# Kernel optimization log

Hardware: AMD Instinct MI355X
Metric: run time of the kernel (lower is better)

The kernel has to match this reference:

```python
import jax, jax.numpy as jnp
import numpy as np

COMMITMENT_COST = 0.25


def setup_inputs() -> dict:
    key = jax.random.key(0)
    k1, k2 = jax.random.split(key)
    z = jax.random.normal(k1, (64, 256, 32, 32), dtype=jnp.float32)
    # codebook init ~ U(-1/K, 1/K) as in torch module
    K, D = 1024, 256
    emb = jax.random.uniform(k2, (K, D), dtype=jnp.float32, minval=-1.0 / K, maxval=1.0 / K)
    return {"z": z, "emb": emb}


def reference(z, emb):
    # b c h w -> b h w c
    zt = jnp.transpose(z, (0, 2, 3, 1))
    B, H, W, C = zt.shape
    zf = zt.reshape(-1, C)  # (b*h*w, c)
    # squared euclidean distances: ||z||^2 + ||e||^2 - 2 z.e
    d = (jnp.sum(zf * zf, axis=1, keepdims=True)
         + jnp.sum(emb * emb, axis=1)
         - 2.0 * jnp.einsum('nd,kd->nk', zf, emb))
    min_encoding_indices = jnp.argmin(d, axis=1)  # (b*h*w,)
    z_quantized = emb[min_encoding_indices].reshape(B, H, W, C)
    commitment_loss = COMMITMENT_COST * jnp.mean((jax.lax.stop_gradient(z_quantized) - zt) ** 2)
    codebook_loss = jnp.mean((z_quantized - jax.lax.stop_gradient(zt)) ** 2)
    loss = commitment_loss + codebook_loss
    # straight-through estimator
    z_quantized = zt + jax.lax.stop_gradient(z_quantized - zt)
    out = jnp.transpose(z_quantized, (0, 3, 1, 2))  # b c h w
    return out, loss, min_encoding_indices.reshape(B, H, W)
```

## Files before the change

### kernel.cpp

```cpp
#include <hip/hip_runtime.h>
#include <math.h>

#define KCODES 1024
#define DDIM   256
#define HWSZ   1024
#define CHW    262144
#define LOSS_OFF 16777216
#define IDX_OFF  16777217
#define TAU_GAP  2e-4f
#define RR4      4

#define WS_ZH   0u
#define WS_EH   33554432u
#define WS_EL   34078720u
#define WS_AN   34603008u
#define WS_BN   34865152u
#define WS_LIST 34869248u
#define WS_CNT  35131392u
#define WS_NEED 35131396u

#define OB_ZH   0
#define OB_EH   8388608
#define OB_EL   8519680
#define OB_AN   8650752
#define OB_BN   8716288
#define OB_LIST 8717312
#define OB_CNT  8782848

typedef __attribute__((ext_vector_type(8))) short short8v;
typedef __attribute__((ext_vector_type(4))) float float4v;

#define GLOAD_LDS(gsrc, ldst)                                                   \
    __builtin_amdgcn_global_load_lds(                                           \
        (const __attribute__((address_space(1))) void*)(gsrc),                  \
        (__attribute__((address_space(3))) void*)(ldst), 16, 0, 0)

static __device__ __forceinline__ unsigned short bf16_rne(float f) {
    unsigned u = __float_as_uint(f);
    return (unsigned short)((u + 0x7FFFu + ((u >> 16) & 1u)) >> 16);
}
static __device__ __forceinline__ float bf16_tf(unsigned short h) {
    return __uint_as_float(((unsigned)h) << 16);
}

__global__ __launch_bounds__(64) void vq_prep_bn(const float* __restrict__ emb,
                                                 float* __restrict__ Bn,
                                                 float* __restrict__ loss_slot,
                                                 int* __restrict__ cnt) {
    int k = blockIdx.x * 64 + threadIdx.x;
    if (k == 0) { *cnt = 0; loss_slot[0] = 0.f; }
    if (k >= KCODES) return;
    const float* e = emb + (size_t)k * DDIM;
    float half[2];
    #pragma unroll
    for (int h = 0; h < 2; ++h) {
        const float* q = e + (h << 7);
        float r[8];
        #pragma unroll
        for (int j = 0; j < 8; ++j) r[j] = __fmul_rn(q[j], q[j]);
        for (int i = 8; i < 128; i += 8) {
            #pragma unroll
            for (int j = 0; j < 8; ++j)
                r[j] = __fadd_rn(r[j], __fmul_rn(q[i + j], q[i + j]));
        }
        half[h] = __fadd_rn(
            __fadd_rn(__fadd_rn(r[0], r[1]), __fadd_rn(r[2], r[3])),
            __fadd_rn(__fadd_rn(r[4], r[5]), __fadd_rn(r[6], r[7])));
    }
    Bn[k] = __fadd_rn(half[0], half[1]);
}

__global__ __launch_bounds__(256) void vq_prep_scatter(const float* __restrict__ emb,
                                                       unsigned short* __restrict__ EHg,
                                                       unsigned short* __restrict__ ELg) {
    int task = blockIdx.x * 256 + threadIdx.x;
    int k  = task >> 5;
    int dg = task & 31;
    const float* e = emb + (size_t)k * DDIM + (dg << 3);
    float4 v0 = *(const float4*)e;
    float4 v1 = *(const float4*)(e + 4);
    float f[8] = {v0.x, v0.y, v0.z, v0.w, v1.x, v1.y, v1.z, v1.w};
    short8v hv, lv;
    #pragma unroll
    for (int j = 0; j < 8; ++j) {
        unsigned short hb = bf16_rne(f[j]);
        unsigned short lb = bf16_rne(f[j] - bf16_tf(hb));
        hv[j] = (short)hb; lv[j] = (short)lb;
    }
    int base = ((k >> 4) << 12) + ((dg >> 2) << 9) + (((k & 15) + ((dg & 3) << 4)) << 3);
    *(short8v*)(EHg + base) = hv;
    *(short8v*)(ELg + base) = lv;
}

__global__ __launch_bounds__(256) void vq_zprep2(const float* __restrict__ z,
                                                 unsigned short* __restrict__ ZHg,
                                                 float* __restrict__ An) {
    __shared__ float hs[2][128];
    const int t = threadIdx.x;
    const int nb = blockIdx.x;
    const int b = nb >> 3, hw0 = (nb & 7) << 7;
    const int h = t >> 7, n = t & 127;
    const float* src = z + (size_t)b * CHW + (size_t)(h << 7) * HWSZ + hw0 + n;
    unsigned short* zbase = ZHg + (size_t)nb * 32768 + ((n >> 4) << 9) + ((n & 15) << 3);
    float r[8];
    #pragma unroll
    for (int blk8 = 0; blk8 < 16; ++blk8) {
        float f[8];
        #pragma unroll
        for (int j = 0; j < 8; ++j) f[j] = src[(size_t)((blk8 << 3) + j) * HWSZ];
        if (blk8 == 0) {
            #pragma unroll
            for (int j = 0; j < 8; ++j) r[j] = __fmul_rn(f[j], f[j]);
        } else {
            #pragma unroll
            for (int j = 0; j < 8; ++j) r[j] = __fadd_rn(r[j], __fmul_rn(f[j], f[j]));
        }
        short8v hv;
        #pragma unroll
        for (int j = 0; j < 8; ++j) hv[j] = (short)bf16_rne(f[j]);
        int d = (h << 7) + (blk8 << 3);
        int s32 = d >> 5, g = (d >> 3) & 3;
        *(short8v*)(zbase + s32 * 4096 + (g << 7)) = hv;
    }
    hs[h][n] = __fadd_rn(
        __fadd_rn(__fadd_rn(r[0], r[1]), __fadd_rn(r[2], r[3])),
        __fadd_rn(__fadd_rn(r[4], r[5]), __fadd_rn(r[6], r[7])));
    __syncthreads();
    if (t < 128) An[nb * 128 + t] = __fadd_rn(hs[0][t], hs[1][t]);
}

template<bool WRITE_OUT>
__global__ __launch_bounds__(512, 4) void vq_argmin2g(
        const unsigned short* __restrict__ ZHg,
        const unsigned short* __restrict__ EHg, const unsigned short* __restrict__ ELg,
        const float* __restrict__ An, const float* __restrict__ Bn,
        float* __restrict__ idx_out, int* __restrict__ list, int* __restrict__ cnt,
        float* __restrict__ loss_slot, float* __restrict__ outp,
        const float* __restrict__ emb) {
    __shared__ uint4 ZH4[512];
    __shared__ uint4 EBUF4[2048];
    __shared__ float BNs[1024];
    unsigned short* ZH = (unsigned short*)ZH4;
    unsigned short* EH = (unsigned short*)EBUF4;
    unsigned short* EL = EH + 8192;

    const int t = threadIdx.x;
    const int bid = blockIdx.x;
    const int nb = ((bid & 7) << 6) + (bid >> 3);
    const int b   = nb >> 3;
    const int hw0 = (nb & 7) << 7;
    const int lane = t & 63, w = t >> 6;
    const int kwv = w >> 1, nwv = w & 1;
    const int l8 = lane << 3, g2 = lane >> 4;

    BNs[t] = Bn[t];
    BNs[t + 512] = Bn[t + 512];

    float an[4];
    #pragma unroll
    for (int nf = 0; nf < 4; ++nf)
        an[nf] = An[nb * 128 + nwv * 64 + nf * 16 + (lane & 15)];

    float mv1[4], mv2[4]; int mi1[4];
    #pragma unroll
    for (int i = 0; i < 4; ++i) { mv1[i] = 3.4e38f; mv2[i] = 3.4e38f; mi1[i] = 0x7fffffff; }

    const uint4* zh4 = (const uint4*)ZHg + (size_t)nb * 4096;
    const uint4* eh4 = (const uint4*)EHg;
    const uint4* el4 = (const uint4*)ELg;

    for (int kt = 0; kt < 4; ++kt) {
        float4v acc[4][4];
        #pragma unroll
        for (int a = 0; a < 4; ++a)
            #pragma unroll
            for (int c = 0; c < 4; ++c) acc[a][c] = (float4v){0.f, 0.f, 0.f, 0.f};

        for (int s32 = 0; s32 < 8; ++s32) {
            __syncthreads();
            GLOAD_LDS(zh4 + s32 * 512 + t, &ZH4[t]);
            #pragma unroll
            for (int p = 0; p < 4; ++p) {
                int s = p * 512 + t;
                int arr = s >> 10, ss = s & 1023;
                const uint4* src = (arr ? el4 : eh4)
                    + (size_t)(((kt << 4) + (ss >> 6)) << 9) + (s32 << 6) + (ss & 63);
                uint4* dst = (arr ? ((uint4*)EL) : ((uint4*)EH)) + ss;
                GLOAD_LDS(src, dst);
            }
            __syncthreads();
            short8v ah[4], al[4], bh[4];
            #pragma unroll
            for (int kf = 0; kf < 4; ++kf) {
                int base = ((kwv * 4 + kf) << 9) + l8;
                ah[kf] = *(const short8v*)&EH[base];
                al[kf] = *(const short8v*)&EL[base];
            }
            #pragma unroll
            for (int nf = 0; nf < 4; ++nf)
                bh[nf] = *(const short8v*)&ZH[((nwv * 4 + nf) << 9) + l8];
            #pragma unroll
            for (int kf = 0; kf < 4; ++kf)
                #pragma unroll
                for (int nf = 0; nf < 4; ++nf) {
                    acc[kf][nf] = __builtin_amdgcn_mfma_f32_16x16x32_bf16(ah[kf], bh[nf], acc[kf][nf], 0, 0, 0);
                    acc[kf][nf] = __builtin_amdgcn_mfma_f32_16x16x32_bf16(al[kf], bh[nf], acc[kf][nf], 0, 0, 0);
                }
        }
        #pragma unroll
        for (int kf = 0; kf < 4; ++kf)
            #pragma unroll
            for (int nf = 0; nf < 4; ++nf)
                #pragma unroll
                for (int r = 0; r < 4; ++r) {
                    int k = kt * 256 + kwv * 64 + kf * 16 + g2 * 4 + r;
                    float s = __fsub_rn(__fadd_rn(an[nf], BNs[k]),
                                        __fmul_rn(2.0f, acc[kf][nf][r]));
                    if (s < mv1[nf] || (s == mv1[nf] && k < mi1[nf])) {
                        mv2[nf] = fminf(mv2[nf], mv1[nf]);
                        mv1[nf] = s; mi1[nf] = k;
                    } else if (s < mv2[nf]) mv2[nf] = s;
                }
    }

    __syncthreads();
    float* REDv = (float*)EBUF4;
    int*   REDi = (int*)((char*)EBUF4 + 8192);
    float* REDw = (float*)((char*)EBUF4 + 16384);
    int*   FIDX = (int*)((char*)EBUF4 + 24576);

    #pragma unroll
    for (int nf = 0; nf < 4; ++nf) {
        int nl = nf * 16 + (lane & 15);
        int slot = kwv * 4 + g2;
        REDv[(nwv * 64 + nl) * 16 + slot] = mv1[nf];
        REDi[(nwv * 64 + nl) * 16 + slot] = mi1[nf];
        REDw[(nwv * 64 + nl) * 16 + slot] = mv2[nf];
    }
    __syncthreads();
    if (t < 128) {
        float bv = 3.4e38f, b2 = 3.4e38f; int bi = 0x7fffffff;
        #pragma unroll
        for (int s = 0; s < 16; ++s) {
            float v1 = REDv[t * 16 + s];
            float v2 = REDw[t * 16 + s];
            int   i1 = REDi[t * 16 + s];
            if (v1 < bv || (v1 == bv && i1 < bi)) { b2 = fminf(b2, bv); bv = v1; bi = i1; }
            else b2 = fminf(b2, v1);
            b2 = fminf(b2, v2);
        }
        int n_glob = nb * 128 + t;
        idx_out[n_glob] = (float)bi;
        FIDX[t] = bi;
        if (b2 - bv < TAU_GAP) {
            int pos = atomicAdd(cnt, 1);
            list[pos] = n_glob;
        }
        float lsum = bv;
        #pragma unroll
        for (int off = 32; off > 0; off >>= 1)
            lsum += __shfl_down(lsum, off, 64);
        if ((t & 63) == 0) atomicAdd(loss_slot, lsum * (1.25f / 16777216.f));
    }
    if (WRITE_OUT) {
        __syncthreads();
        int n_loc = t & 127, cg = t >> 7;
        int idx = FIDX[n_loc];
        int hw = hw0 + n_loc;
        const float4* erow = (const float4*)(emb + (size_t)idx * DDIM + (cg << 6));
        float* obase = outp + (size_t)b * CHW + (size_t)(cg << 6) * HWSZ + hw;
        #pragma unroll 4
        for (int q = 0; q < 16; ++q) {
            float4 v = erow[q];
            obase[(size_t)(q * 4 + 0) * HWSZ] = v.x;
            obase[(size_t)(q * 4 + 1) * HWSZ] = v.y;
            obase[(size_t)(q * 4 + 2) * HWSZ] = v.z;
            obase[(size_t)(q * 4 + 3) * HWSZ] = v.w;
        }
    }
}

template<bool WRITE_OUT>
__global__ __launch_bounds__(512) void vq_rescore_c(
        const float* __restrict__ z, const float* __restrict__ emb,
        const float* __restrict__ An, const float* __restrict__ Bn,
        float* __restrict__ idx_out, const int* __restrict__ list,
        const int* __restrict__ cnt, float* __restrict__ outp) {
    const int c = *cnt;
    const int t = threadIdx.x;
    const int lane = t & 63, w = t >> 6;
    const int g  = lane >> 4;
    const int ch = lane & 15;
    __shared__ float zs[RR4][256];
    __shared__ float Ars[RR4];
    __shared__ int   rid[RR4];
    __shared__ float wsv[RR4][8];
    __shared__ int   wsi[RR4][8];
    __shared__ int   wbi[RR4];

    for (int base = blockIdx.x * RR4; base < c; base += gridDim.x * RR4) {
        const int nrows = min(RR4, c - base);
        __syncthreads();
        if (t < nrows) { int n = list[base + t]; rid[t] = n; Ars[t] = An[n]; }
        __syncthreads();
        for (int i = t; i < (nrows << 8); i += 512) {
            int r = i >> 8, d = i & 255;
            int n = rid[r];
            zs[r][d] = z[(size_t)(n >> 10) * CHW + (size_t)d * HWSZ + (n & 1023)];
        }
        __syncthreads();

        float bv[RR4]; int bi[RR4];
        #pragma unroll
        for (int r = 0; r < RR4; ++r) { bv[r] = 3.4e38f; bi[r] = 0x7fffffff; }

        for (int p = 0; p < 32; ++p) {
            int cc = p * 32 + w * 4 + g;
            const float4* e4 = (const float4*)(emb + (size_t)cc * DDIM);
            double part[RR4];
            #pragma unroll
            for (int r = 0; r < RR4; ++r) part[r] = 0.0;
            #pragma unroll
            for (int it = 0; it < 4; ++it) {
                float4 ev = e4[it * 16 + ch];
                #pragma unroll
                for (int r = 0; r < RR4; ++r) {
                    float4 zv = *(const float4*)&zs[r][(it * 16 + ch) << 2];
                    part[r] += (double)ev.x * zv.x + (double)ev.y * zv.y
                             + (double)ev.z * zv.z + (double)ev.w * zv.w;
                }
            }
            #pragma unroll
            for (int off = 1; off <= 8; off <<= 1)
                #pragma unroll
                for (int r = 0; r < RR4; ++r)
                    part[r] += __shfl_xor(part[r], off, 64);
            float Bk = Bn[cc];
            #pragma unroll
            for (int r = 0; r < RR4; ++r) {
                float s = __fsub_rn(__fadd_rn(Ars[r], Bk),
                                    __fmul_rn(2.0f, (float)part[r]));
                if (s < bv[r]) { bv[r] = s; bi[r] = cc; }
            }
        }
        #pragma unroll
        for (int r = 0; r < RR4; ++r) {
            float v = bv[r]; int i1 = bi[r];
            #pragma unroll
            for (int off = 16; off <= 32; off <<= 1) {
                float ov = __shfl_xor(v, off, 64);
                int   oi = __shfl_xor(i1, off, 64);
                if (ov < v || (ov == v && oi < i1)) { v = ov; i1 = oi; }
            }
            if (lane == 0) { wsv[r][w] = v; wsi[r][w] = i1; }
        }
        __syncthreads();
        if (t < nrows) {
            float v = wsv[t][0]; int i1 = wsi[t][0];
            #pragma unroll
            for (int j = 1; j < 8; ++j) {
                float ov = wsv[t][j]; int oi = wsi[t][j];
                if (ov < v || (ov == v && oi < i1)) { v = ov; i1 = oi; }
            }
            idx_out[rid[t]] = (float)i1;
            wbi[t] = i1;
        }
        if (WRITE_OUT) {
            __syncthreads();
            for (int i = t; i < (nrows << 8); i += 512) {
                int r = i >> 8, d = i & 255;
                int n = rid[r];
                outp[(size_t)(n >> 10) * CHW + (size_t)d * HWSZ + (n & 1023)]
                    = emb[(size_t)wbi[r] * DDIM + d];
            }
        }
    }
}

__global__ __launch_bounds__(256) void vq_epilogue(const float* __restrict__ emb,
                                                   float* __restrict__ outp,
                                                   const float* __restrict__ idxf) {
    const int t  = threadIdx.x;
    const int nc = blockIdx.x;
    const int b  = nc >> 4;
    const int hw = ((nc & 15) << 6) + (t & 63);
    const int n  = (b << 10) + hw;
    const int idx = (int)idxf[n];
    const float* erow = emb + (size_t)idx * DDIM;
    const size_t zb = (size_t)b * CHW + hw;

    const int cbase = (t >> 6) << 2;
    #pragma unroll 4
    for (int cq = 0; cq < 16; ++cq) {
        int c = cbase + (cq << 4);
        float4 q4 = *reinterpret_cast<const float4*>(erow + c);
        outp[zb + (size_t)(c + 0) * HWSZ] = q4.x;
        outp[zb + (size_t)(c + 1) * HWSZ] = q4.y;
        outp[zb + (size_t)(c + 2) * HWSZ] = q4.z;
        outp[zb + (size_t)(c + 3) * HWSZ] = q4.w;
    }
}

extern "C" void kernel_launch(void* const* d_in, const int* in_sizes, int n_in,
                              void* d_out, int out_size, void* d_ws, size_t ws_size,
                              hipStream_t stream) {
    const float* z   = (const float*)d_in[0];
    const float* emb = (const float*)d_in[1];
    float* out       = (float*)d_out;
    float* loss_slot = out + LOSS_OFF;
    float* idx_out   = out + IDX_OFF;

    if (ws_size >= (size_t)WS_NEED) {
        char* ws = (char*)d_ws;
        unsigned short* ZHg = (unsigned short*)(ws + WS_ZH);
        unsigned short* EHg = (unsigned short*)(ws + WS_EH);
        unsigned short* ELg = (unsigned short*)(ws + WS_EL);
        float* An = (float*)(ws + WS_AN);
        float* Bn = (float*)(ws + WS_BN);
        int*  list = (int*)(ws + WS_LIST);
        int*  cnt  = (int*)(ws + WS_CNT);

        vq_prep_bn          <<<dim3(16),   dim3(64),  0, stream>>>(emb, Bn, loss_slot, cnt);
        vq_prep_scatter     <<<dim3(128),  dim3(256), 0, stream>>>(emb, EHg, ELg);
        vq_zprep2           <<<dim3(512),  dim3(256), 0, stream>>>(z, ZHg, An);
        vq_argmin2g<true>   <<<dim3(512),  dim3(512), 0, stream>>>(ZHg, EHg, ELg, An, Bn,
                                 idx_out, list, cnt, loss_slot, out, emb);
        vq_rescore_c<true>  <<<dim3(2048), dim3(512), 0, stream>>>(z, emb, An, Bn,
                                 idx_out, list, cnt, out);
    } else {
        unsigned short* ZHg = (unsigned short*)(out + OB_ZH);
        unsigned short* EHg = (unsigned short*)(out + OB_EH);
        unsigned short* ELg = (unsigned short*)(out + OB_EL);
        float* An = out + OB_AN;
        float* Bn = out + OB_BN;
        int*  list = (int*)(out + OB_LIST);
        int*  cnt  = (int*)(out + OB_CNT);

        vq_prep_bn          <<<dim3(16),   dim3(64),  0, stream>>>(emb, Bn, loss_slot, cnt);
        vq_prep_scatter     <<<dim3(128),  dim3(256), 0, stream>>>(emb, EHg, ELg);
        vq_zprep2           <<<dim3(512),  dim3(256), 0, stream>>>(z, ZHg, An);
        vq_argmin2g<false>  <<<dim3(512),  dim3(512), 0, stream>>>(ZHg, EHg, ELg, An, Bn,
                                 idx_out, list, cnt, loss_slot, out, emb);
        vq_rescore_c<false> <<<dim3(2048), dim3(512), 0, stream>>>(z, emb, An, Bn,
                                 idx_out, list, cnt, out);
        vq_epilogue         <<<dim3(1024), dim3(256), 0, stream>>>(emb, out, idx_out);
    }
}
```

Measured before the change: 256.9 us.

## Double-buffer codebook tiles and keep full Z tile resident in LDS

The argmin kernel now loads the entire 128-row bf16 Z tile into shared memory once and double-buffers the codebook hi/lo chunks, so each chunk's global-to-LDS load for the next step overlaps the MFMA work on the current one. This cuts the barrier count per step from two to one. Shared memory per block rises to about 132 KB and launch bounds drop to 2 blocks per CU, which lowers occupancy. The tie-gap threshold for sending rows to the exact rescoring pass is also tightened, so fewer rows are rescored, at some risk of missing near-tie argmins.

```diff
diff --git a/kernel.cpp b/kernel.cpp
--- a/kernel.cpp
+++ b/kernel.cpp
@@ -7,7 +7,7 @@
 #define CHW    262144
 #define LOSS_OFF 16777216
 #define IDX_OFF  16777217
-#define TAU_GAP  2e-4f
+#define TAU_GAP  1.4e-4f
 #define RR4      4
 
 #define WS_ZH   0u
@@ -130,19 +130,17 @@
 }
 
 template<bool WRITE_OUT>
-__global__ __launch_bounds__(512, 4) void vq_argmin2g(
+__global__ __launch_bounds__(512, 2) void vq_argmin2p(
         const unsigned short* __restrict__ ZHg,
         const unsigned short* __restrict__ EHg, const unsigned short* __restrict__ ELg,
         const float* __restrict__ An, const float* __restrict__ Bn,
         float* __restrict__ idx_out, int* __restrict__ list, int* __restrict__ cnt,
         float* __restrict__ loss_slot, float* __restrict__ outp,
         const float* __restrict__ emb) {
-    __shared__ uint4 ZH4[512];
-    __shared__ uint4 EBUF4[2048];
+    __shared__ uint4 ZA4[4096];
+    __shared__ uint4 EB4[2][2048];
     __shared__ float BNs[1024];
-    unsigned short* ZH = (unsigned short*)ZH4;
-    unsigned short* EH = (unsigned short*)EBUF4;
-    unsigned short* EL = EH + 8192;
+    unsigned short* ZA = (unsigned short*)ZA4;
 
     const int t = threadIdx.x;
     const int bid = blockIdx.x;
@@ -153,81 +151,96 @@
     const int kwv = w >> 1, nwv = w & 1;
     const int l8 = lane << 3, g2 = lane >> 4;
 
-    BNs[t] = Bn[t];
-    BNs[t + 512] = Bn[t + 512];
-
-    float an[4];
-    #pragma unroll
-    for (int nf = 0; nf < 4; ++nf)
-        an[nf] = An[nb * 128 + nwv * 64 + nf * 16 + (lane & 15)];
-
-    float mv1[4], mv2[4]; int mi1[4];
-    #pragma unroll
-    for (int i = 0; i < 4; ++i) { mv1[i] = 3.4e38f; mv2[i] = 3.4e38f; mi1[i] = 0x7fffffff; }
-
     const uint4* zh4 = (const uint4*)ZHg + (size_t)nb * 4096;
     const uint4* eh4 = (const uint4*)EHg;
     const uint4* el4 = (const uint4*)ELg;
 
-    for (int kt = 0; kt < 4; ++kt) {
-        float4v acc[4][4];
-        #pragma unroll
-        for (int a = 0; a < 4; ++a)
-            #pragma unroll
-            for (int c = 0; c < 4; ++c) acc[a][c] = (float4v){0.f, 0.f, 0.f, 0.f};
-
-        for (int s32 = 0; s32 < 8; ++s32) {
-            __syncthreads();
-            GLOAD_LDS(zh4 + s32 * 512 + t, &ZH4[t]);
+    #pragma unroll
+    for (int p = 0; p < 8; ++p)
+        GLOAD_LDS(zh4 + p * 512 + t, &ZA4[p * 512 + t]);
+    #pragma unroll
+    for (int p = 0; p < 4; ++p) {
+        int s = p * 512 + t;
+        int arr = s >> 10, ss = s & 1023;
+        const uint4* src = (arr ? el4 : eh4)
+            + (size_t)((ss >> 6) << 9) + (ss & 63);
+        GLOAD_LDS(src, &EB4[0][arr * 1024 + ss]);
+    }
+    BNs[t] = Bn[t];
+    BNs[t + 512] = Bn[t + 512];
+    float an[4];
+    #pragma unroll
+    for (int nf = 0; nf < 4; ++nf)
+        an[nf] = An[nb * 128 + nwv * 64 + nf * 16 + (lane & 15)];
+
+    float mv1[4], mv2[4]; int mi1[4];
+    #pragma unroll
+    for (int i = 0; i < 4; ++i) { mv1[i] = 3.4e38f; mv2[i] = 3.4e38f; mi1[i] = 0x7fffffff; }
+
+    __syncthreads();
+
+    float4v acc[4][4];
+    for (int c = 0; c < 32; ++c) {
+        const int kt = c >> 3, s32 = c & 7, cur = c & 1;
+        if (s32 == 0) {
+            #pragma unroll
+            for (int a = 0; a < 4; ++a)
+                #pragma unroll
+                for (int q = 0; q < 4; ++q) acc[a][q] = (float4v){0.f, 0.f, 0.f, 0.f};
+        }
+        if (c < 31) {
+            const int c2 = c + 1, kt2 = c2 >> 3, s2 = c2 & 7;
             #pragma unroll
             for (int p = 0; p < 4; ++p) {
                 int s = p * 512 + t;
                 int arr = s >> 10, ss = s & 1023;
                 const uint4* src = (arr ? el4 : eh4)
-                    + (size_t)(((kt << 4) + (ss >> 6)) << 9) + (s32 << 6) + (ss & 63);
-                uint4* dst = (arr ? ((uint4*)EL) : ((uint4*)EH)) + ss;
-                GLOAD_LDS(src, dst);
-            }
-            __syncthreads();
-            short8v ah[4], al[4], bh[4];
-            #pragma unroll
-            for (int kf = 0; kf < 4; ++kf) {
-                int base = ((kwv * 4 + kf) << 9) + l8;
-                ah[kf] = *(const short8v*)&EH[base];
-                al[kf] = *(const short8v*)&EL[base];
-            }
-            #pragma unroll
-            for (int nf = 0; nf < 4; ++nf)
-                bh[nf] = *(const short8v*)&ZH[((nwv * 4 + nf) << 9) + l8];
+                    + (size_t)(((kt2 << 4) + (ss >> 6)) << 9) + (s2 << 6) + (ss & 63);
+                GLOAD_LDS(src, &EB4[cur ^ 1][arr * 1024 + ss]);
+            }
+        }
+        const unsigned short* EHc = (const unsigned short*)EB4[cur];
+        const unsigned short* ELc = EHc + 8192;
+        short8v ah[4], al[4], bh[4];
+        #pragma unroll
+        for (int kf = 0; kf < 4; ++kf) {
+            int base = ((kwv * 4 + kf) << 9) + l8;
+            ah[kf] = *(const short8v*)&EHc[base];
+            al[kf] = *(const short8v*)&ELc[base];
+        }
+        #pragma unroll
+        for (int nf = 0; nf < 4; ++nf)
+            bh[nf] = *(const short8v*)&ZA[(s32 << 12) + ((nwv * 4 + nf) << 9) + l8];
+        #pragma unroll
+        for (int kf = 0; kf < 4; ++kf)
+            #pragma unroll
+            for (int nf = 0; nf < 4; ++nf) {
+                acc[kf][nf] = __builtin_amdgcn_mfma_f32_16x16x32_bf16(ah[kf], bh[nf], acc[kf][nf], 0, 0, 0);
+                acc[kf][nf] = __builtin_amdgcn_mfma_f32_16x16x32_bf16(al[kf], bh[nf], acc[kf][nf], 0, 0, 0);
+            }
+        if (s32 == 7) {
             #pragma unroll
             for (int kf = 0; kf < 4; ++kf)
                 #pragma unroll
-                for (int nf = 0; nf < 4; ++nf) {
-                    acc[kf][nf] = __builtin_amdgcn_mfma_f32_16x16x32_bf16(ah[kf], bh[nf], acc[kf][nf], 0, 0, 0);
-                    acc[kf][nf] = __builtin_amdgcn_mfma_f32_16x16x32_bf16(al[kf], bh[nf], acc[kf][nf], 0, 0, 0);
-                }
-        }
-        #pragma unroll
-        for (int kf = 0; kf < 4; ++kf)
-            #pragma unroll
-            for (int nf = 0; nf < 4; ++nf)
-                #pragma unroll
-                for (int r = 0; r < 4; ++r) {
-                    int k = kt * 256 + kwv * 64 + kf * 16 + g2 * 4 + r;
-                    float s = __fsub_rn(__fadd_rn(an[nf], BNs[k]),
-                                        __fmul_rn(2.0f, acc[kf][nf][r]));
-                    if (s < mv1[nf] || (s == mv1[nf] && k < mi1[nf])) {
-                        mv2[nf] = fminf(mv2[nf], mv1[nf]);
-                        mv1[nf] = s; mi1[nf] = k;
-                    } else if (s < mv2[nf]) mv2[nf] = s;
-                }
-    }
-
-    __syncthreads();
-    float* REDv = (float*)EBUF4;
-    int*   REDi = (int*)((char*)EBUF4 + 8192);
-    float* REDw = (float*)((char*)EBUF4 + 16384);
-    int*   FIDX = (int*)((char*)EBUF4 + 24576);
+                for (int nf = 0; nf < 4; ++nf)
+                    #pragma unroll
+                    for (int r = 0; r < 4; ++r) {
+                        int k = kt * 256 + kwv * 64 + kf * 16 + g2 * 4 + r;
+                        float s = __fsub_rn(__fadd_rn(an[nf], BNs[k]),
+                                            __fmul_rn(2.0f, acc[kf][nf][r]));
+                        if (s < mv1[nf] || (s == mv1[nf] && k < mi1[nf])) {
+                            mv2[nf] = fminf(mv2[nf], mv1[nf]);
+                            mv1[nf] = s; mi1[nf] = k;
+                        } else if (s < mv2[nf]) mv2[nf] = s;
+                    }
+        }
+        __syncthreads();
+    }
+
+    float* REDv = (float*)EB4;
+    int*   REDi = (int*)((char*)EB4 + 8192);
+    float* REDw = (float*)((char*)EB4 + 16384);
+    int*   FIDX = (int*)((char*)EB4 + 24576);
 
     #pragma unroll
     for (int nf = 0; nf < 4; ++nf) {
@@ -423,7 +436,7 @@
         vq_prep_bn          <<<dim3(16),   dim3(64),  0, stream>>>(emb, Bn, loss_slot, cnt);
         vq_prep_scatter     <<<dim3(128),  dim3(256), 0, stream>>>(emb, EHg, ELg);
         vq_zprep2           <<<dim3(512),  dim3(256), 0, stream>>>(z, ZHg, An);
-        vq_argmin2g<true>   <<<dim3(512),  dim3(512), 0, stream>>>(ZHg, EHg, ELg, An, Bn,
+        vq_argmin2p<true>   <<<dim3(512),  dim3(512), 0, stream>>>(ZHg, EHg, ELg, An, Bn,
                                  idx_out, list, cnt, loss_slot, out, emb);
         vq_rescore_c<true>  <<<dim3(2048), dim3(512), 0, stream>>>(z, emb, An, Bn,
                                  idx_out, list, cnt, out);
@@ -439,7 +452,7 @@
         vq_prep_bn          <<<dim3(16),   dim3(64),  0, stream>>>(emb, Bn, loss_slot, cnt);
         vq_prep_scatter     <<<dim3(128),  dim3(256), 0, stream>>>(emb, EHg, ELg);
         vq_zprep2           <<<dim3(512),  dim3(256), 0, stream>>>(z, ZHg, An);
-        vq_argmin2g<false>  <<<dim3(512),  dim3(512), 0, stream>>>(ZHg, EHg, ELg, An, Bn,
+        vq_argmin2p<false>  <<<dim3(512),  dim3(512), 0, stream>>>(ZHg, EHg, ELg, An, Bn,
                                  idx_out, list, cnt, loss_slot, out, emb);
         vq_rescore_c<false> <<<dim3(2048), dim3(512), 0, stream>>>(z, emb, An, Bn,
                                  idx_out, list, cnt, out);
```

Result: slower. 268.2 us (+4.4%).
